# Kernel tuning notes

Measured on AMD Instinct MI355X. Metric: run time of the kernel, lower is better.

Reference implementation:

```python
import jax, jax.numpy as jnp
import numpy as np

NUM_CLASSES = 3
BBOX_W, OBJ_W, CLS_W = 0.05, 1.0, 0.5


def setup_inputs() -> dict:
    key = jax.random.key(0)
    kp, kc, kcl, kv = jax.random.split(key, 4)
    B, C, H, W, N = 64, 8, 256, 256, 200
    pred = jax.random.normal(kp, (B, C, H, W), dtype=jnp.float32)
    # normalized (x, y, w, h) in (0, 1) so every label is in-bounds with positive coord sum
    coords = jax.random.uniform(kc, (B, N, 4), jnp.float32, 1e-3, 0.999)
    cls_id = jax.random.randint(kcl, (B, N), 0, NUM_CLASSES).astype(jnp.float32)
    invalid = jax.random.uniform(kv, (B, N)) < 0.25
    cls_id = jnp.where(invalid, -1.0, cls_id)
    targets = jnp.concatenate([cls_id[..., None], coords], axis=-1)  # [B, N, 5]
    return {"pred": pred, "targets": targets}


def _bce_with_logits(logits, z):
    # stable: softplus(x) - x*z  ==  max(x,0) - x*z + log(1+exp(-|x|))
    return jax.nn.softplus(logits) - logits * z


def reference(pred, targets):
    B, C, H, W = pred.shape
    cls_id = targets[..., 0]            # [B, N]
    coords = targets[..., 1:5]          # [B, N, 4] = (x, y, w, h)

    valid = (cls_id >= 0) & (coords.sum(-1) > 0)
    # int() truncation of x*w / y*h (coords nonnegative -> floor)
    xpix = (coords[..., 0] * W).astype(jnp.int32)
    ypix = (coords[..., 1] * H).astype(jnp.int32)
    in_bounds = (xpix >= 0) & (xpix < W) & (ypix >= 0) & (ypix < H)
    mask = (valid & in_bounds).astype(pred.dtype)   # [B, N]

    xs = jnp.clip(xpix, 0, W - 1)
    ys = jnp.clip(ypix, 0, H - 1)
    bidx = jnp.arange(B)[:, None]
    # gather pred[b, :, y, x] for every label -> [B, N, C]
    p = pred[bidx, :, ys, xs]

    # bbox: MSE mean over the 4 coords (torch detaches target_coords via torch.tensor())
    tgt = jax.lax.stop_gradient(coords)
    bbox = jnp.mean((p[..., :4] - tgt) ** 2, axis=-1)            # [B, N]
    # objectness: BCEWithLogits against 1.0 (mean over 1 element)
    obj = _bce_with_logits(p[..., 4], 1.0)                       # [B, N]
    # class: BCEWithLogits against one-hot(class_id), mean over classes
    onehot = jax.nn.one_hot(jnp.clip(cls_id, 0, None).astype(jnp.int32),
                            NUM_CLASSES, dtype=pred.dtype)       # [B, N, K]
    cls_l = jnp.mean(_bce_with_logits(p[..., 5:5 + NUM_CLASSES], onehot), axis=-1)

    bbox_sum = jnp.sum(bbox * mask)
    obj_sum = jnp.sum(obj * mask)
    cls_sum = jnp.sum(cls_l * mask)
    total = BBOX_W * bbox_sum + OBJ_W * obj_sum + CLS_W * cls_sum
    # (total, bbox, obj, cls) matching the dict values of the torch module
    return jnp.stack([total, bbox_sum, obj_sum, cls_sum])
```

## Files before the change

kernel.cpp:

```cpp
#include <hip/hip_runtime.h>
#include <math.h>

#define BD 64
#define ND 200
#define CD 8
#define HD 256
#define WD 256
#define NBOX (BD * ND)
#define NBLK (NBOX / 256)

__device__ __forceinline__ float softplus_f(float x) {
    return fmaxf(x, 0.0f) + log1pf(expf(-fabsf(x)));
}

__global__ __launch_bounds__(256) void yolo_partial(const float* __restrict__ pred,
                                                    const float* __restrict__ targets,
                                                    float* __restrict__ partial) {
    const int tid = blockIdx.x * 256 + threadIdx.x;
    const int b = tid / ND;

    const float* t = targets + (size_t)tid * 5;
    const float cls_id = t[0];
    const float c0 = t[1], c1 = t[2], c2 = t[3], c3 = t[4];

    const bool valid = (cls_id >= 0.0f) && ((c0 + c1 + c2 + c3) > 0.0f);
    const int xpix = (int)(c0 * (float)WD);
    const int ypix = (int)(c1 * (float)HD);
    const bool inb = (xpix >= 0) && (xpix < WD) && (ypix >= 0) && (ypix < HD);
    const bool m = valid && inb;

    float bbox = 0.0f, obj = 0.0f, clsl = 0.0f;
    if (m) {
        const int xs = min(max(xpix, 0), WD - 1);
        const int ys = min(max(ypix, 0), HD - 1);
        const float* pb = pred + (size_t)b * CD * HD * WD + (size_t)ys * WD + xs;
        float p[8];
#pragma unroll
        for (int c = 0; c < 8; ++c) p[c] = pb[(size_t)c * (HD * WD)];

        const float d0 = p[0] - c0, d1 = p[1] - c1, d2 = p[2] - c2, d3 = p[3] - c3;
        bbox = 0.25f * (d0 * d0 + d1 * d1 + d2 * d2 + d3 * d3);
        obj = softplus_f(p[4]) - p[4];

        const int ci = (int)fmaxf(cls_id, 0.0f);
        float s = 0.0f;
#pragma unroll
        for (int k = 0; k < 3; ++k) {
            const float z = (k == ci) ? 1.0f : 0.0f;
            s += softplus_f(p[5 + k]) - p[5 + k] * z;
        }
        clsl = s * (1.0f / 3.0f);
    }

#pragma unroll
    for (int off = 32; off > 0; off >>= 1) {
        bbox += __shfl_down(bbox, off, 64);
        obj  += __shfl_down(obj,  off, 64);
        clsl += __shfl_down(clsl, off, 64);
    }

    __shared__ float sb[4], so[4], sc[4];
    const int wave = threadIdx.x >> 6;
    const int lane = threadIdx.x & 63;
    if (lane == 0) { sb[wave] = bbox; so[wave] = obj; sc[wave] = clsl; }
    __syncthreads();

    if (threadIdx.x == 0) {
        partial[blockIdx.x * 3 + 0] = sb[0] + sb[1] + sb[2] + sb[3];
        partial[blockIdx.x * 3 + 1] = so[0] + so[1] + so[2] + so[3];
        partial[blockIdx.x * 3 + 2] = sc[0] + sc[1] + sc[2] + sc[3];
    }
}

__global__ __launch_bounds__(64) void yolo_final(const float* __restrict__ partial,
                                                 float* __restrict__ out) {
    const int t = threadIdx.x;
    float tb = 0.0f, to = 0.0f, tc = 0.0f;
    if (t < NBLK) {
        tb = partial[t * 3 + 0];
        to = partial[t * 3 + 1];
        tc = partial[t * 3 + 2];
    }
#pragma unroll
    for (int off = 32; off > 0; off >>= 1) {
        tb += __shfl_down(tb, off, 64);
        to += __shfl_down(to, off, 64);
        tc += __shfl_down(tc, off, 64);
    }
    if (t == 0) {
        out[0] = 0.05f * tb + 1.0f * to + 0.5f * tc;
        out[1] = tb;
        out[2] = to;
        out[3] = tc;
    }
}

extern "C" void kernel_launch(void* const* d_in, const int* in_sizes, int n_in,
                              void* d_out, int out_size, void* d_ws, size_t ws_size,
                              hipStream_t stream) {
    const float* pred    = (const float*)d_in[0];
    const float* targets = (const float*)d_in[1];
    float* out     = (float*)d_out;
    float* partial = (float*)d_ws;

    yolo_partial<<<NBLK, 256, 0, stream>>>(pred, targets, partial);
    yolo_final<<<1, 64, 0, stream>>>(partial, out);
}
```

Baseline: 166.4 us.

## Split each box's channel gathers across eight threads

Each box is now handled by eight threads, one per channel, instead of one thread issuing eight serial strided loads. The aim is more parallelism and more outstanding memory requests for the latency-bound random gather, since the original launch had only 50 blocks. The final reduction grows to 256 threads with a strided loop to absorb the 400 partials. In exchange, the targets row is loaded redundantly by each of the eight threads, and the softplus branches now diverge within a wave.

```diff
diff --git a/kernel.cpp b/kernel.cpp
--- a/kernel.cpp
+++ b/kernel.cpp
@@ -6,8 +6,10 @@
 #define CD 8
 #define HD 256
 #define WD 256
+#define HW (HD * WD)
 #define NBOX (BD * ND)
-#define NBLK (NBOX / 256)
+#define NTHR (NBOX * CD)
+#define NBLK (NTHR / 256)
 
 __device__ __forceinline__ float softplus_f(float x) {
     return fmaxf(x, 0.0f) + log1pf(expf(-fabsf(x)));
@@ -17,9 +19,11 @@
                                                     const float* __restrict__ targets,
                                                     float* __restrict__ partial) {
     const int tid = blockIdx.x * 256 + threadIdx.x;
-    const int b = tid / ND;
+    const int box = tid >> 3;
+    const int c   = tid & 7;
+    const int b   = box / ND;
 
-    const float* t = targets + (size_t)tid * 5;
+    const float* t = targets + (size_t)box * 5;
     const float cls_id = t[0];
     const float c0 = t[1], c1 = t[2], c2 = t[3], c3 = t[4];
 
@@ -33,23 +37,19 @@
     if (m) {
         const int xs = min(max(xpix, 0), WD - 1);
         const int ys = min(max(ypix, 0), HD - 1);
-        const float* pb = pred + (size_t)b * CD * HD * WD + (size_t)ys * WD + xs;
-        float p[8];
-#pragma unroll
-        for (int c = 0; c < 8; ++c) p[c] = pb[(size_t)c * (HD * WD)];
+        const float p = pred[(size_t)b * CD * HW + (size_t)c * HW + (size_t)ys * WD + xs];
 
-        const float d0 = p[0] - c0, d1 = p[1] - c1, d2 = p[2] - c2, d3 = p[3] - c3;
-        bbox = 0.25f * (d0 * d0 + d1 * d1 + d2 * d2 + d3 * d3);
-        obj = softplus_f(p[4]) - p[4];
-
-        const int ci = (int)fmaxf(cls_id, 0.0f);
-        float s = 0.0f;
-#pragma unroll
-        for (int k = 0; k < 3; ++k) {
-            const float z = (k == ci) ? 1.0f : 0.0f;
-            s += softplus_f(p[5 + k]) - p[5 + k] * z;
+        if (c < 4) {
+            const float tc = (c == 0) ? c0 : (c == 1) ? c1 : (c == 2) ? c2 : c3;
+            const float d = p - tc;
+            bbox = 0.25f * d * d;
+        } else if (c == 4) {
+            obj = softplus_f(p) - p;
+        } else {
+            const int ci = (int)fmaxf(cls_id, 0.0f);
+            const float z = ((c - 5) == ci) ? 1.0f : 0.0f;
+            clsl = (softplus_f(p) - p * z) * (1.0f / 3.0f);
         }
-        clsl = s * (1.0f / 3.0f);
     }
 
 #pragma unroll
@@ -72,14 +72,14 @@
     }
 }
 
-__global__ __launch_bounds__(64) void yolo_final(const float* __restrict__ partial,
-                                                 float* __restrict__ out) {
+__global__ __launch_bounds__(256) void yolo_final(const float* __restrict__ partial,
+                                                  float* __restrict__ out) {
     const int t = threadIdx.x;
     float tb = 0.0f, to = 0.0f, tc = 0.0f;
-    if (t < NBLK) {
-        tb = partial[t * 3 + 0];
-        to = partial[t * 3 + 1];
-        tc = partial[t * 3 + 2];
+    for (int i = t; i < NBLK; i += 256) {
+        tb += partial[i * 3 + 0];
+        to += partial[i * 3 + 1];
+        tc += partial[i * 3 + 2];
     }
 #pragma unroll
     for (int off = 32; off > 0; off >>= 1) {
@@ -87,11 +87,20 @@
         to += __shfl_down(to, off, 64);
         tc += __shfl_down(tc, off, 64);
     }
+    __shared__ float sb[4], so[4], sc[4];
+    const int wave = t >> 6;
+    const int lane = t & 63;
+    if (lane == 0) { sb[wave] = tb; so[wave] = to; sc[wave] = tc; }
+    __syncthreads();
+
     if (t == 0) {
-        out[0] = 0.05f * tb + 1.0f * to + 0.5f * tc;
-        out[1] = tb;
-        out[2] = to;
-        out[3] = tc;
+        const float B = sb[0] + sb[1] + sb[2] + sb[3];
+        const float O = so[0] + so[1] + so[2] + so[3];
+        const float C = sc[0] + sc[1] + sc[2] + sc[3];
+        out[0] = 0.05f * B + 1.0f * O + 0.5f * C;
+        out[1] = B;
+        out[2] = O;
+        out[3] = C;
     }
 }
 
@@ -104,5 +113,5 @@
     float* partial = (float*)d_ws;
 
     yolo_partial<<<NBLK, 256, 0, stream>>>(pred, targets, partial);
-    yolo_final<<<1, 64, 0, stream>>>(partial, out);
+    yolo_final<<<1, 256, 0, stream>>>(partial, out);
 }
```

New measurement: 164.7 us. No clear change (-1.0%).
